# Optimization experiments

Measured on AMD Instinct MI355X. Metric: run time of the kernel, lower is better.

The kernel has to match this reference:

```python
import jax, jax.numpy as jnp
import numpy as np

N = 6            # ensemble members (must match share_mode '6-1')
IN_C = 128
OUT_C = 128
K = 3
STRIDE = 1
PAD = 1
D = IN_C * OUT_C * K * K  # 147456
TEMP = 1.0
ZP1 = 1.2
ZP2 = -0.2
RES_DENOS = (3.0, 5.0)   # res_denos[:maxBWPow] with bw=2 -> [2**2-1, 2**2+1]


def round_ste(v):
    # straight-through round: forward round, backward identity
    return v + jax.lax.stop_gradient(jnp.round(v) - v)


def setup_inputs() -> dict:
    key = jax.random.key(0)
    k1, k2, k3, k4 = jax.random.split(key, 4)
    x = jax.random.normal(k1, (48, IN_C, 64, 64), jnp.float32)
    U = jax.random.normal(k2, (N, D), jnp.float32)
    bp = jax.random.normal(k3, (N + 1, D), jnp.float32)
    # uniform noise for the gumbel-sigmoid sample (open interval to avoid log(0))
    u = jax.random.uniform(k4, (N + 1, D), jnp.float32, 1e-6, 1.0 - 1e-6)
    return {"x": x, "U": U, "bp": bp, "u": u}


def reference(x, U, bp, u):
    beta = jnp.max(U)
    alpha = jnp.min(U)

    # gumbel-sigmoid gating
    g = jnp.log(u / (1.0 - u))
    bsamples = jax.nn.sigmoid((g + bp) / TEMP)
    gates = jnp.clip(bsamples * (ZP1 - ZP2) + ZP2, 0.0, 1.0)  # (7, D)
    # first 6 rows: per-member gates for level 0; last row shared across members for level 1
    gates = jnp.stack([gates[:N], jnp.broadcast_to(gates[N:], (N, D))], axis=0)  # (2, N, D)
    order_gates = jax.lax.stop_gradient(
        jnp.cumprod((gates > 0).astype(gates.dtype), axis=0)
    )

    # sequential residual-bit STE quantization (2 levels)
    s1 = (beta - alpha) / RES_DENOS[0]
    v1 = s1 * round_ste(U / s1)                       # (N, D)
    s2 = s1 / RES_DENOS[1]
    v2 = s2 * round_ste((U - v1.mean(0)) / s2)        # (N, D); vals.sum(0).mean(0) == v1.mean(0)
    vals = jnp.stack([v1, v2], axis=0)                # (2, N, D)

    w = (vals * (gates * order_gates)).sum(0)         # (N, D)
    w = w.reshape(OUT_C * N, IN_C, K, K)

    B = x.shape[0]
    xr = x.reshape(B // N, N * x.shape[1], x.shape[2], x.shape[3])
    act = jax.lax.conv_general_dilated(
        xr, w,
        window_strides=(STRIDE, STRIDE),
        padding=[(PAD, PAD), (PAD, PAD)],
        dimension_numbers=('NCHW', 'OIHW', 'NCHW'),
        feature_group_count=N,
    )
    return act.reshape(act.shape[0] * N, act.shape[1] // N, act.shape[2], act.shape[3])
```

## Files before the change

### kernel.cpp

```cpp
#include <hip/hip_runtime.h>
#include <stdint.h>

typedef __attribute__((ext_vector_type(8))) short bf16x8;
typedef __attribute__((ext_vector_type(4))) float f32x4;

#define DW 147456
#define NTOT (6 * DW)

__device__ __forceinline__ unsigned short f2bf(float f) {
    unsigned int u = __float_as_uint(f);
    u = (u + 0x7FFFu + ((u >> 16) & 1u)) >> 16;
    return (unsigned short)u;
}

__global__ __launch_bounds__(256) void reduce_part(const float* __restrict__ U,
                                                   float* __restrict__ part) {
    int tid = threadIdx.x;
    float mx = -INFINITY, mn = INFINITY;
    const float4* U4 = (const float4*)U;
    for (int i = blockIdx.x * 256 + tid; i < NTOT / 4; i += 256 * 256) {
        float4 v = U4[i];
        mx = fmaxf(fmaxf(fmaxf(mx, v.x), v.y), fmaxf(v.z, v.w));
        mn = fminf(fminf(fminf(mn, v.x), v.y), fminf(v.z, v.w));
    }
    __shared__ float smx[256], smn[256];
    smx[tid] = mx; smn[tid] = mn;
    __syncthreads();
    for (int s = 128; s > 0; s >>= 1) {
        if (tid < s) {
            smx[tid] = fmaxf(smx[tid], smx[tid + s]);
            smn[tid] = fminf(smn[tid], smn[tid + s]);
        }
        __syncthreads();
    }
    if (tid == 0) { part[blockIdx.x] = smx[0]; part[256 + blockIdx.x] = smn[0]; }
}

__global__ __launch_bounds__(256) void make_weights(const float* __restrict__ U,
                                                    const float* __restrict__ bp,
                                                    const float* __restrict__ uu,
                                                    const float* __restrict__ part,
                                                    unsigned short* __restrict__ Wb2) {
    int tid = threadIdx.x;
    __shared__ float smx[256], smn[256];
    smx[tid] = part[tid]; smn[tid] = part[256 + tid];
    __syncthreads();
    for (int s = 128; s > 0; s >>= 1) {
        if (tid < s) {
            smx[tid] = fmaxf(smx[tid], smx[tid + s]);
            smn[tid] = fminf(smn[tid], smn[tid + s]);
        }
        __syncthreads();
    }
    float beta = smx[0], alpha = smn[0];
    float s1 = (beta - alpha) / 3.0f;
    float s2 = s1 / 5.0f;

    int d = blockIdx.x * 256 + tid;

    float v1[6]; float Uv[6]; float vsum = 0.f;
    #pragma unroll
    for (int n = 0; n < 6; n++) {
        float Un = U[n * DW + d];
        Uv[n] = Un;
        float v = s1 * rintf(Un / s1);
        v1[n] = v; vsum += v;
    }
    float vmean = vsum / 6.0f;

    float g6;
    {
        float un = uu[6 * DW + d];
        float sg = un / (un + (1.0f - un) * expf(-bp[6 * DW + d]));
        g6 = fminf(fmaxf(sg * 1.4f - 0.2f, 0.0f), 1.0f);
    }

    int oc = d / 1152;
    int rem = d - oc * 1152;
    int ic = rem / 9;
    int t9 = rem - ic * 9;
    int c = ic >> 5, icc = ic & 31;
    int och = oc >> 6, ocl = oc & 63;
    int mi = ocl >> 4, lrr = ocl & 15;
    int lq = icc >> 3, jj = icc & 7;
    size_t base = ((size_t)(c * 2 + och) * 9 + t9) * 2048
                + (size_t)mi * 512 + (size_t)(lq * 16 + lrr) * 8 + jj;

    #pragma unroll
    for (int n = 0; n < 6; n++) {
        float un = uu[n * DW + d];
        float sg = un / (un + (1.0f - un) * expf(-bp[n * DW + d]));
        float g0 = fminf(fmaxf(sg * 1.4f - 0.2f, 0.0f), 1.0f);
        float v2 = s2 * rintf((Uv[n] - vmean) / s2);
        float w = v1[n] * g0 + ((g0 > 0.0f && g6 > 0.0f) ? v2 * g6 : 0.0f);
        Wb2[(size_t)n * DW + base] = f2bf(w);
    }
}

__global__ __launch_bounds__(256) void transform_x(const float* __restrict__ x,
                                                   unsigned short* __restrict__ xT) {
    __shared__ unsigned short Sh[128 * 70];
    int b = blockIdx.x;
    int img = b >> 6, row = b & 63;
    int tid = threadIdx.x;
    {
        int ch = tid >> 1;
        int col0 = (tid & 1) * 32;
        const float* src = x + (((size_t)(img * 128 + ch) * 64 + row) * 64 + col0);
        #pragma unroll
        for (int j = 0; j < 8; j++) {
            float4 v = ((const float4*)src)[j];
            unsigned int p0 = (unsigned int)f2bf(v.x) | ((unsigned int)f2bf(v.y) << 16);
            unsigned int p1 = (unsigned int)f2bf(v.z) | ((unsigned int)f2bf(v.w) << 16);
            unsigned int* dst = (unsigned int*)&Sh[ch * 70 + col0 + j * 4];
            dst[0] = p0; dst[1] = p1;
        }
    }
    __syncthreads();
    {
        int col = tid & 63;
        int q = tid >> 6;
        int chg = q * 32;
        int h = ((col + 1) >> 1) & 3;
        union { unsigned short s[32]; uint4 v[4]; } tmp;
        #pragma unroll
        for (int j = 0; j < 32; j++) tmp.s[j] = Sh[(chg + j) * 70 + col];
        uint4* dst = (uint4*)(xT + ((size_t)img * 524288 + (size_t)q * 131072 +
                                    (size_t)row * 2048 + col * 32));
        #pragma unroll
        for (int k = 0; k < 4; k++) dst[k] = tmp.v[k ^ h];
    }
}

typedef const __attribute__((address_space(1))) void CGV;
typedef __attribute__((address_space(3))) void LV;

__global__ __launch_bounds__(256, 2) void conv_mfma(const unsigned short* __restrict__ xT,
                                                    const unsigned short* __restrict__ Wb2,
                                                    float* __restrict__ out) {
    __shared__ __align__(16) unsigned short Xs[6 * 66 * 32];
    __shared__ __align__(16) unsigned short Ws[9 * 64 * 32];
    int o = blockIdx.x;
    int blk = (o & 7) * 192 + (o >> 3);
    int band = blk & 15;
    int och = (blk >> 4) & 1;
    int img = blk >> 5;
    int row0 = band * 4;
    int mem = img - (img / 6) * 6;
    const unsigned short* Wmem = Wb2 + (size_t)mem * DW;
    const unsigned short* Xsrc = xT + (size_t)img * 524288;

    int tid = threadIdx.x;
    int lane = tid & 63;
    int prow = tid >> 6;
    int lr = lane & 15, lq = lane >> 4;
    int so0 = (lq ^ ((lr >> 1) & 3)) * 8;
    int so1 = (lq ^ (((lr + 1) >> 1) & 3)) * 8;
    int so2 = (lq ^ (((lr + 2) >> 1) & 3)) * 8;

    if (tid < 192) {
        int r = tid >> 5, j = tid & 31;
        int col = (j < 16) ? 0 : 65;
        *(unsigned int*)&Xs[(r * 66 + col) * 32 + (j & 15) * 2] = 0u;
    }

    auto stage = [&](int c) {
        const unsigned short* wsrc = Wmem + (size_t)((c * 2 + och) * 9) * 2048;
        #pragma unroll
        for (int t = 0; t < 9; t++)
            __builtin_amdgcn_global_load_lds((CGV*)(wsrc + t * 2048 + tid * 8),
                                             (LV*)(&Ws[t * 2048 + tid * 8]), 16, 0, 0);
        #pragma unroll
        for (int r = 0; r < 6; r++) {
            int srow = row0 + r - 1;
            if ((unsigned)srow < 64u)
                __builtin_amdgcn_global_load_lds((CGV*)(Xsrc + c * 131072 + srow * 2048 + tid * 8),
                                                 (LV*)(&Xs[(r * 66 + 1) * 32 + tid * 8]), 16, 0, 0);
            else
                *(uint4*)&Xs[(r * 66 + 1) * 32 + tid * 8] = make_uint4(0u, 0u, 0u, 0u);
        }
    };

    f32x4 acc[4][4];
    #pragma unroll
    for (int mi = 0; mi < 4; mi++)
        #pragma unroll
        for (int ni = 0; ni < 4; ni++)
            acc[mi][ni] = (f32x4){0.f, 0.f, 0.f, 0.f};

    stage(0);
    __syncthreads();

    for (int c = 0; c < 4; c++) {
        #pragma unroll
        for (int t = 0; t < 9; t++) {
            const int dy = t / 3, dx = t - (t / 3) * 3;
            const int so = (dx == 0) ? so0 : (dx == 1) ? so1 : so2;
            bf16x8 af[4], bfr[4];
            #pragma unroll
            for (int mi = 0; mi < 4; mi++)
                af[mi] = *(const bf16x8*)(&Ws[t * 2048 + mi * 512 + lane * 8]);
            #pragma unroll
            for (int ni = 0; ni < 4; ni++) {
                int col = ni * 16 + lr + dx;
                bfr[ni] = *(const bf16x8*)(&Xs[((prow + dy) * 66 + col) * 32 + so]);
            }
            #pragma unroll
            for (int mi = 0; mi < 4; mi++)
                #pragma unroll
                for (int ni = 0; ni < 4; ni++)
                    acc[mi][ni] = __builtin_amdgcn_mfma_f32_16x16x32_bf16(
                        af[mi], bfr[ni], acc[mi][ni], 0, 0, 0);
        }
        if (c < 3) {
            __syncthreads();
            stage(c + 1);
            __syncthreads();
        }
    }

    float* obase = out + (size_t)img * 524288 + (size_t)(row0 + prow) * 64;
    #pragma unroll
    for (int mi = 0; mi < 4; mi++) {
        #pragma unroll
        for (int ni = 0; ni < 4; ni++) {
            int px = ni * 16 + lr;
            int ocb = och * 64 + mi * 16 + lq * 4;
            #pragma unroll
            for (int rr = 0; rr < 4; rr++)
                obase[(size_t)(ocb + rr) * 4096 + px] = acc[mi][ni][rr];
        }
    }
}

extern "C" void kernel_launch(void* const* d_in, const int* in_sizes, int n_in,
                              void* d_out, int out_size, void* d_ws, size_t ws_size,
                              hipStream_t stream) {
    const float* x  = (const float*)d_in[0];
    const float* U  = (const float*)d_in[1];
    const float* bp = (const float*)d_in[2];
    const float* uu = (const float*)d_in[3];
    float* out = (float*)d_out;

    char* ws = (char*)d_ws;
    float* part = (float*)ws;
    unsigned short* Wb2 = (unsigned short*)(ws + 4096);
    unsigned short* xT  = (unsigned short*)(ws + 4096 + 1769472);

    reduce_part <<<256, 256, 0, stream>>>(U, part);
    make_weights<<<576, 256, 0, stream>>>(U, bp, uu, part, Wb2);
    transform_x <<<48 * 64, 256, 0, stream>>>(x, xT);
    conv_mfma   <<<48 * 32, 256, 0, stream>>>(xT, Wb2, out);
}
```

Before: 266.5 us.

## Fuse x bf16 conversion into conv kernel with register-prefetched staging

Removes the separate transform_x kernel and its bf16 intermediate. The conv kernel now reads fp32 x directly, converts it to bf16 and writes it into LDS with a swizzle. Global loads for the next channel chunk go into registers before the MFMA loop, so they overlap compute instead of using direct-to-LDS loads after a barrier. This saves a kernel launch and a full read/write of the transformed x. In exchange it adds register pressure (about 84 extra VGPRs for prefetch) and reads x from overlapping halo rows several times, in fp32.

```diff
diff --git a/kernel.cpp b/kernel.cpp
--- a/kernel.cpp
+++ b/kernel.cpp
@@ -97,45 +97,7 @@
     }
 }
 
-__global__ __launch_bounds__(256) void transform_x(const float* __restrict__ x,
-                                                   unsigned short* __restrict__ xT) {
-    __shared__ unsigned short Sh[128 * 70];
-    int b = blockIdx.x;
-    int img = b >> 6, row = b & 63;
-    int tid = threadIdx.x;
-    {
-        int ch = tid >> 1;
-        int col0 = (tid & 1) * 32;
-        const float* src = x + (((size_t)(img * 128 + ch) * 64 + row) * 64 + col0);
-        #pragma unroll
-        for (int j = 0; j < 8; j++) {
-            float4 v = ((const float4*)src)[j];
-            unsigned int p0 = (unsigned int)f2bf(v.x) | ((unsigned int)f2bf(v.y) << 16);
-            unsigned int p1 = (unsigned int)f2bf(v.z) | ((unsigned int)f2bf(v.w) << 16);
-            unsigned int* dst = (unsigned int*)&Sh[ch * 70 + col0 + j * 4];
-            dst[0] = p0; dst[1] = p1;
-        }
-    }
-    __syncthreads();
-    {
-        int col = tid & 63;
-        int q = tid >> 6;
-        int chg = q * 32;
-        int h = ((col + 1) >> 1) & 3;
-        union { unsigned short s[32]; uint4 v[4]; } tmp;
-        #pragma unroll
-        for (int j = 0; j < 32; j++) tmp.s[j] = Sh[(chg + j) * 70 + col];
-        uint4* dst = (uint4*)(xT + ((size_t)img * 524288 + (size_t)q * 131072 +
-                                    (size_t)row * 2048 + col * 32));
-        #pragma unroll
-        for (int k = 0; k < 4; k++) dst[k] = tmp.v[k ^ h];
-    }
-}
-
-typedef const __attribute__((address_space(1))) void CGV;
-typedef __attribute__((address_space(3))) void LV;
-
-__global__ __launch_bounds__(256, 2) void conv_mfma(const unsigned short* __restrict__ xT,
+__global__ __launch_bounds__(256, 2) void conv_mfma(const float* __restrict__ x,
                                                     const unsigned short* __restrict__ Wb2,
                                                     float* __restrict__ out) {
     __shared__ __align__(16) unsigned short Xs[6 * 66 * 32];
@@ -148,15 +110,21 @@
     int row0 = band * 4;
     int mem = img - (img / 6) * 6;
     const unsigned short* Wmem = Wb2 + (size_t)mem * DW;
-    const unsigned short* Xsrc = xT + (size_t)img * 524288;
 
     int tid = threadIdx.x;
     int lane = tid & 63;
-    int prow = tid >> 6;
+    int g = tid >> 6;
+    int prow = g;
     int lr = lane & 15, lq = lane >> 4;
+    int q = lane & 31;
+    int rsub = lane >> 5;
     int so0 = (lq ^ ((lr >> 1) & 3)) * 8;
     int so1 = (lq ^ (((lr + 1) >> 1) & 3)) * 8;
     int so2 = (lq ^ (((lr + 2) >> 1) & 3)) * 8;
+    int ws0 = (g ^ (q & 3)) * 8;
+    int ws1 = (g ^ ((q + 1) & 3)) * 8;
+
+    const float* xg = x + ((size_t)img * 128 + g * 8) * 4096 + 2 * q;
 
     if (tid < 192) {
         int r = tid >> 5, j = tid & 31;
@@ -164,20 +132,46 @@
         *(unsigned int*)&Xs[(r * 66 + col) * 32 + (j & 15) * 2] = 0u;
     }
 
-    auto stage = [&](int c) {
-        const unsigned short* wsrc = Wmem + (size_t)((c * 2 + och) * 9) * 2048;
+    float2 xv[3][8];
+    uint4 wv[9];
+
+    auto issue_loads = [&](int c) {
+        const unsigned short* wsrc = Wmem + (size_t)((c * 2 + och) * 9) * 2048 + tid * 8;
         #pragma unroll
         for (int t = 0; t < 9; t++)
-            __builtin_amdgcn_global_load_lds((CGV*)(wsrc + t * 2048 + tid * 8),
-                                             (LV*)(&Ws[t * 2048 + tid * 8]), 16, 0, 0);
-        #pragma unroll
-        for (int r = 0; r < 6; r++) {
-            int srow = row0 + r - 1;
-            if ((unsigned)srow < 64u)
-                __builtin_amdgcn_global_load_lds((CGV*)(Xsrc + c * 131072 + srow * 2048 + tid * 8),
-                                                 (LV*)(&Xs[(r * 66 + 1) * 32 + tid * 8]), 16, 0, 0);
-            else
-                *(uint4*)&Xs[(r * 66 + 1) * 32 + tid * 8] = make_uint4(0u, 0u, 0u, 0u);
+            wv[t] = *(const uint4*)(wsrc + t * 2048);
+        #pragma unroll
+        for (int it = 0; it < 3; it++) {
+            int srow = row0 + it * 2 + rsub - 1;
+            bool ok = (unsigned)srow < 64u;
+            const float* rp = xg + (size_t)c * 131072 + srow * 64;
+            #pragma unroll
+            for (int k = 0; k < 8; k++) {
+                float2 v = ok ? *(const float2*)(rp + k * 4096) : float2{0.f, 0.f};
+                xv[it][k] = v;
+            }
+        }
+    };
+
+    auto pack_write = [&]() {
+        #pragma unroll
+        for (int t = 0; t < 9; t++)
+            *(uint4*)&Ws[t * 2048 + tid * 8] = wv[t];
+        #pragma unroll
+        for (int it = 0; it < 3; it++) {
+            int r = it * 2 + rsub;
+            unsigned int d0[4], d1[4];
+            #pragma unroll
+            for (int d = 0; d < 4; d++) {
+                d0[d] = (unsigned int)f2bf(xv[it][2 * d].x) |
+                        ((unsigned int)f2bf(xv[it][2 * d + 1].x) << 16);
+                d1[d] = (unsigned int)f2bf(xv[it][2 * d].y) |
+                        ((unsigned int)f2bf(xv[it][2 * d + 1].y) << 16);
+            }
+            *(uint4*)&Xs[(r * 66 + 1 + 2 * q) * 32 + ws0] =
+                make_uint4(d0[0], d0[1], d0[2], d0[3]);
+            *(uint4*)&Xs[(r * 66 + 2 + 2 * q) * 32 + ws1] =
+                make_uint4(d1[0], d1[1], d1[2], d1[3]);
         }
     };
 
@@ -188,10 +182,12 @@
         for (int ni = 0; ni < 4; ni++)
             acc[mi][ni] = (f32x4){0.f, 0.f, 0.f, 0.f};
 
-    stage(0);
+    issue_loads(0);
+    pack_write();
     __syncthreads();
 
     for (int c = 0; c < 4; c++) {
+        if (c < 3) issue_loads(c + 1);
         #pragma unroll
         for (int t = 0; t < 9; t++) {
             const int dy = t / 3, dx = t - (t / 3) * 3;
@@ -214,7 +210,7 @@
         }
         if (c < 3) {
             __syncthreads();
-            stage(c + 1);
+            pack_write();
             __syncthreads();
         }
     }
@@ -245,10 +241,8 @@
     char* ws = (char*)d_ws;
     float* part = (float*)ws;
     unsigned short* Wb2 = (unsigned short*)(ws + 4096);
-    unsigned short* xT  = (unsigned short*)(ws + 4096 + 1769472);
 
     reduce_part <<<256, 256, 0, stream>>>(U, part);
     make_weights<<<576, 256, 0, stream>>>(U, bp, uu, part, Wb2);
-    transform_x <<<48 * 64, 256, 0, stream>>>(x, xT);
-    conv_mfma   <<<48 * 32, 256, 0, stream>>>(xT, Wb2, out);
-}
+    conv_mfma   <<<48 * 32, 256, 0, stream>>>(x, Wb2, out);
+}
```

Measured after the change: 322.0 us. +20.8%, slower.
